# Performance work log

Hardware: AMD Instinct MI355X
Metric: run time of the kernel (lower is better)

Reference implementation:

```python
import jax, jax.numpy as jnp
import numpy as np

B, C, Hf, Wf, HM, P = 64, 2048, 16, 16, 256, 10  # P = num_parts, NP = graph nodes
NP = P - 1
EPS = 1e-5  # BatchNorm eps

def bn_eval(x, g, b, rm, rv):
    return (x - rm) * jax.lax.rsqrt(rv + EPS) * g + b

def setup_inputs() -> dict:
    key = jax.random.key(0)
    ks = jax.random.split(key, 6)
    return {
        "x_global": jax.random.normal(ks[0], (B, C, Hf, Wf), jnp.float32),
        "x_gcn": jax.random.normal(ks[1], (B, C, Hf, Wf), jnp.float32),
        "mask": jax.random.randint(ks[2], (B, 1, HM, HM), 0, P, jnp.int32),
        "adj": jax.random.uniform(ks[3], (B, NP, NP), jnp.float32),
        "W1": jax.random.normal(ks[4], (C, C), jnp.float32) * 0.02,
        "b1": jnp.zeros((C,), jnp.float32),
        "g1": jnp.ones((NP * C,), jnp.float32), "be1": jnp.zeros((NP * C,), jnp.float32),
        "rm1": jnp.zeros((NP * C,), jnp.float32), "rv1": jnp.ones((NP * C,), jnp.float32),
        "W2": jax.random.normal(ks[5], (C, C), jnp.float32) * 0.02,
        "b2": jnp.zeros((C,), jnp.float32),
        "g2": jnp.ones((NP * C,), jnp.float32), "be2": jnp.zeros((NP * C,), jnp.float32),
        "rm2": jnp.zeros((NP * C,), jnp.float32), "rv2": jnp.ones((NP * C,), jnp.float32),
        "gb_g": jnp.ones((C,), jnp.float32), "gb_b": jnp.zeros((C,), jnp.float32),
        "gb_rm": jnp.zeros((C,), jnp.float32), "gb_rv": jnp.ones((C,), jnp.float32),
        "gn_g": jnp.ones((C,), jnp.float32), "gn_b": jnp.zeros((C,), jnp.float32),
        "gn_rm": jnp.zeros((C,), jnp.float32), "gn_rv": jnp.ones((C,), jnp.float32),
    }

def gc_layer(x, adj, Wt, bias, g, be, rm, rv):
    # GraphConvolution: matmul -> bmm(adj) -> bias -> BN over flattened (B, NP*C)
    s = jnp.einsum('bpc,cd->bpd', x, Wt)
    o = jnp.einsum('bpq,bqd->bpd', adj, s) + bias
    flat = o.reshape(o.shape[0], -1)
    return bn_eval(flat, g, be, rm, rv).reshape(o.shape)

def reference(x_global, x_gcn, mask, adj, W1, b1, g1, be1, rm1, rv1,
              W2, b2, g2, be2, rm2, rv2, gb_g, gb_b, gb_rm, gb_rv,
              gn_g, gn_b, gn_rm, gn_rv):
    # --- global branch: GAP + bottleneck BN (eval) ---
    feat_global = x_global.mean(axis=(2, 3))                      # (B, C)
    bnfeat_global = bn_eval(feat_global, gb_g, gb_b, gb_rm, gb_rv)

    # --- nearest-neighbor downsample of mask to feature-map size ---
    stride = HM // Hf
    mr = mask[:, 0, ::stride, ::stride]                           # (B, h, w)

    # one-hot part masks for classes 1..P-1: (B, h, w, NP)
    onehot = (mr[..., None] == jnp.arange(1, P)).astype(jnp.float32)
    counts = onehot.sum(axis=(1, 2))                              # (B, NP)

    # deterministic part dropout: drop the first present part per image
    drop = jnp.argmax(counts > 0, axis=1) + 1                     # (B,)
    keep = (mr != drop[:, None, None]).astype(jnp.float32)        # (B, h, w)
    x_self = x_gcn * keep[:, None, :, :]

    # segment mean pooling per part: (B, NP, C)
    denom = (counts + 1e-8)[..., None]
    mask_feat = jnp.einsum('bchw,bhwp->bpc', x_gcn, onehot) / denom
    self_feat = jnp.einsum('bchw,bhwp->bpc', x_self, onehot) / denom

    def gcn(x):
        x1 = jax.nn.relu(gc_layer(x, adj, W1, b1, g1, be1, rm1, rv1))
        x2 = jax.nn.relu(gc_layer(x1, adj, W2, b2, g2, be2, rm2, rv2))
        return x2.mean(axis=1), x2.reshape(x2.shape[0], -1)

    feat_gcn, feat_gcn_cat = gcn(mask_feat)
    feat_self, feat_self_cat = gcn(self_feat)
    bnfeat_gcn = bn_eval(feat_gcn, gn_g, gn_b, gn_rm, gn_rv)
    bnfeat_self = bn_eval(feat_self, gn_g, gn_b, gn_rm, gn_rv)

    # concatenate eval-mode outputs into one array: (B, 3*C + 2*NP*C)
    return jnp.concatenate([bnfeat_global, bnfeat_gcn, bnfeat_self,
                            feat_gcn_cat, feat_self_cat], axis=1)
```

## Files before the change

kernel.cpp:

```cpp
#include <hip/hip_runtime.h>
#include <cstdint>
#include <cstddef>

#define EPSV 1e-5f

typedef __bf16 bf16x8 __attribute__((ext_vector_type(8)));
typedef float f32x4 __attribute__((ext_vector_type(4)));

__device__ __forceinline__ unsigned short f2bf(float f) {
  unsigned int u = __float_as_uint(f);
  u += 0x7FFFu + ((u >> 16) & 1u);
  return (unsigned short)(u >> 16);
}

__device__ __forceinline__ void async_copy16(const void* src, void* dst_lds) {
  __builtin_amdgcn_global_load_lds(
      (const __attribute__((address_space(1))) void*)src,
      (__attribute__((address_space(3))) void*)dst_lds, 16, 0, 0);
}

__global__ __launch_bounds__(256) void kmean(
    const float* __restrict__ x, const float* __restrict__ g,
    const float* __restrict__ bb, const float* __restrict__ rm,
    const float* __restrict__ rv, float* __restrict__ out) {
  int gw = blockIdx.x * 4 + (threadIdx.x >> 6);
  int lane = threadIdx.x & 63;
  float4 v = ((const float4*)(x + (size_t)gw * 256))[lane];
  float s = v.x + v.y + v.z + v.w;
#pragma unroll
  for (int o = 32; o > 0; o >>= 1) s += __shfl_xor(s, o, 64);
  if (lane == 0) {
    int b = gw >> 11, c = gw & 2047;
    float m = s * (1.f / 256.f);
    out[(size_t)b * 43008 + c] =
        (m - rm[c]) / sqrtf(rv[c] + EPSV) * g[c] + bb[c];
  }
}

__global__ __launch_bounds__(256) void kmask(
    const int* __restrict__ mask, int* __restrict__ partid,
    float* __restrict__ invden, int* __restrict__ dropm1) {
  int b = blockIdx.x;
  int t = threadIdx.x;
  int h = t >> 4, w = t & 15;
  int m = mask[(size_t)b * 65536 + h * 4096 + w * 16];
  partid[b * 256 + t] = m;
  __shared__ int cnt[10];
  if (t < 10) cnt[t] = 0;
  __syncthreads();
  atomicAdd(&cnt[m], 1);
  __syncthreads();
  if (t == 0) {
    int dp = 0;
    for (int p = 8; p >= 0; p--)
      if (cnt[p + 1] > 0) dp = p;
    dropm1[b] = dp;
  }
  if (t < 9) invden[b * 9 + t] = 1.f / ((float)cnt[t + 1] + 1e-8f);
}

__global__ __launch_bounds__(256) void kpool_mfma(
    const float* __restrict__ x, const int* __restrict__ partid,
    const float* __restrict__ invden, const int* __restrict__ dropm1,
    unsigned short* __restrict__ Abuf) {
  __shared__ unsigned short As[64 * 264];
  __shared__ unsigned short Bs[16 * 264];
  __shared__ int pid[256];
  const int t = threadIdx.x;
  const int b = blockIdx.y;
  const int c0 = blockIdx.x * 64;

  pid[t] = partid[b * 256 + t];

  const float4* xg = (const float4*)(x + ((size_t)(b * 2048 + c0)) * 256);
#pragma unroll
  for (int it = 0; it < 16; it++) {
    int idx = t + it * 256;
    float4 v = xg[idx];
    int row = idx >> 6, sc = (idx & 63) * 4;
    ushort4 h;
    h.x = f2bf(v.x); h.y = f2bf(v.y); h.z = f2bf(v.z); h.w = f2bf(v.w);
    *(ushort4*)&As[row * 264 + sc] = h;
  }
  __syncthreads();
  {
    int p = t >> 4, s0 = (t & 15) * 16;
#pragma unroll
    for (int j = 0; j < 16; j++)
      Bs[p * 264 + s0 + j] =
          (pid[s0 + j] == p + 1) ? (unsigned short)0x3F80 : (unsigned short)0;
  }
  __syncthreads();

  const int wave = t >> 6;
  const int l16 = t & 15;
  const int quad = (t & 63) >> 4;
  f32x4 acc = (f32x4){0.f, 0.f, 0.f, 0.f};
#pragma unroll
  for (int ks = 0; ks < 8; ks++) {
    bf16x8 a = *(const bf16x8*)&As[(wave * 16 + l16) * 264 + ks * 32 + quad * 8];
    bf16x8 bf = *(const bf16x8*)&Bs[l16 * 264 + ks * 32 + quad * 8];
    acc = __builtin_amdgcn_mfma_f32_16x16x32_bf16(a, bf, acc, 0, 0, 0);
  }

  if (l16 < 9) {
    int p = l16;
    float inv = invden[b * 9 + p];
    int dm1 = dropm1[b];
    int cbase = c0 + wave * 16 + quad * 4;
    ushort4 hm;
    hm.x = f2bf(acc[0] * inv);
    hm.y = f2bf(acc[1] * inv);
    hm.z = f2bf(acc[2] * inv);
    hm.w = f2bf(acc[3] * inv);
    ushort4 hs = (p == dm1) ? (ushort4){0, 0, 0, 0} : hm;
    *(ushort4*)&Abuf[(size_t)(b * 9 + p) * 2048 + cbase] = hm;
    *(ushort4*)&Abuf[(size_t)((64 + b) * 9 + p) * 2048 + cbase] = hs;
  }
}

__global__ __launch_bounds__(256) void ktranspose(
    const float* __restrict__ W1, const float* __restrict__ W2,
    unsigned short* __restrict__ Wt1, unsigned short* __restrict__ Wt2) {
  const float* W = blockIdx.z ? W2 : W1;
  unsigned short* Wt = blockIdx.z ? Wt2 : Wt1;
  __shared__ float tile[32][33];
  int tx = threadIdx.x & 31;
  int ty = threadIdx.x >> 5;
  int k0 = blockIdx.y * 32;
  int n0 = blockIdx.x * 32;
#pragma unroll
  for (int i = 0; i < 32; i += 8)
    tile[ty + i][tx] = W[(size_t)(k0 + ty + i) * 2048 + n0 + tx];
  __syncthreads();
#pragma unroll
  for (int i = 0; i < 32; i += 8)
    Wt[(size_t)(n0 + ty + i) * 2048 + k0 + tx] = f2bf(tile[tx][ty + i]);
}

#define GK 2048
__global__ __launch_bounds__(256) void gemm_bf16(
    const unsigned short* __restrict__ A, const unsigned short* __restrict__ Bt,
    float* __restrict__ S) {
  __shared__ unsigned short As[128 * 32];
  __shared__ unsigned short Bs[128 * 32];
  const int tid = threadIdx.x;
  const int lane = tid & 63;
  const int wave = tid >> 6;
  const int wm = (wave >> 1) << 6;
  const int wn = (wave & 1) << 6;
  const int quad = lane >> 4;
  const int l16 = lane & 15;
  const int by = blockIdx.y;
  const int bx = blockIdx.x;
  const int kz = blockIdx.z;

  const unsigned short* Ag = A + (size_t)by * 128 * GK;
  const unsigned short* Bg = Bt + (size_t)bx * 128 * GK;
  S += (size_t)kz * 1152 * 2048;

  f32x4 acc[4][4];
#pragma unroll
  for (int i = 0; i < 4; i++)
#pragma unroll
    for (int j = 0; j < 4; j++) acc[i][j] = (f32x4){0.f, 0.f, 0.f, 0.f};

  const int seg0 = tid, seg1 = tid + 256;
  const int r0 = seg0 >> 2, c0 = (seg0 & 3) * 8;
  const int r1 = seg1 >> 2, c1 = (seg1 & 3) * 8;

  const int kbeg = kz * (GK / 2), kend = kbeg + (GK / 2);
  for (int kk = kbeg; kk < kend; kk += 32) {
    __syncthreads();
    async_copy16(Ag + (size_t)r0 * GK + kk + c0, &As[seg0 * 8]);
    async_copy16(Ag + (size_t)r1 * GK + kk + c1, &As[seg1 * 8]);
    async_copy16(Bg + (size_t)r0 * GK + kk + c0, &Bs[seg0 * 8]);
    async_copy16(Bg + (size_t)r1 * GK + kk + c1, &Bs[seg1 * 8]);
    asm volatile("s_waitcnt vmcnt(0)" ::: "memory");
    __syncthreads();

    bf16x8 af[4], bfr[4];
#pragma unroll
    for (int i = 0; i < 4; i++)
      af[i] = *(const bf16x8*)&As[(wm + i * 16 + l16) * 32 + quad * 8];
#pragma unroll
    for (int j = 0; j < 4; j++)
      bfr[j] = *(const bf16x8*)&Bs[(wn + j * 16 + l16) * 32 + quad * 8];
#pragma unroll
    for (int i = 0; i < 4; i++)
#pragma unroll
      for (int j = 0; j < 4; j++)
        acc[i][j] = __builtin_amdgcn_mfma_f32_16x16x32_bf16(af[i], bfr[j],
                                                            acc[i][j], 0, 0, 0);
  }

#pragma unroll
  for (int i = 0; i < 4; i++)
#pragma unroll
    for (int j = 0; j < 4; j++)
#pragma unroll
      for (int r = 0; r < 4; r++) {
        int m = by * 128 + wm + i * 16 + quad * 4 + r;
        int n = bx * 128 + wn + j * 16 + l16;
        S[(size_t)m * 2048 + n] = acc[i][j][r];
      }
}

__global__ __launch_bounds__(256) void epi_mid(
    const float* __restrict__ S0, const float* __restrict__ S1,
    const float* __restrict__ adj, const float* __restrict__ bias,
    const float* __restrict__ g, const float* __restrict__ be,
    const float* __restrict__ rm, const float* __restrict__ rv,
    unsigned short* __restrict__ Aout) {
  int idx = blockIdx.x * 256 + threadIdx.x;
  int d = idx & 2047;
  int bb = idx >> 11;
  int b = bb & 63;
  float s[9];
#pragma unroll
  for (int q = 0; q < 9; q++) {
    size_t off = (size_t)(bb * 9 + q) * 2048 + d;
    s[q] = S0[off] + S1[off];
  }
#pragma unroll
  for (int p = 0; p < 9; p++) {
    float o = bias[d];
#pragma unroll
    for (int q = 0; q < 9; q++) o += adj[b * 81 + p * 9 + q] * s[q];
    int f = p * 2048 + d;
    float v = (o - rm[f]) / sqrtf(rv[f] + EPSV) * g[f] + be[f];
    v = fmaxf(v, 0.f);
    Aout[(size_t)(bb * 9 + p) * 2048 + d] = f2bf(v);
  }
}

__global__ __launch_bounds__(256) void epi_final(
    const float* __restrict__ S0, const float* __restrict__ S1,
    const float* __restrict__ adj, const float* __restrict__ bias,
    const float* __restrict__ g, const float* __restrict__ be,
    const float* __restrict__ rm, const float* __restrict__ rv,
    const float* __restrict__ gn_g, const float* __restrict__ gn_b,
    const float* __restrict__ gn_rm, const float* __restrict__ gn_rv,
    float* __restrict__ out) {
  int idx = blockIdx.x * 256 + threadIdx.x;
  int d = idx & 2047;
  int bb = idx >> 11;
  int b = bb & 63;
  bool selfb = bb >= 64;
  float s[9];
#pragma unroll
  for (int q = 0; q < 9; q++) {
    size_t off = (size_t)(bb * 9 + q) * 2048 + d;
    s[q] = S0[off] + S1[off];
  }
  float* orow = out + (size_t)b * 43008;
  size_t catbase = selfb ? 24576 : 6144;
  float mean = 0.f;
#pragma unroll
  for (int p = 0; p < 9; p++) {
    float o = bias[d];
#pragma unroll
    for (int q = 0; q < 9; q++) o += adj[b * 81 + p * 9 + q] * s[q];
    int f = p * 2048 + d;
    float v = (o - rm[f]) / sqrtf(rv[f] + EPSV) * g[f] + be[f];
    v = fmaxf(v, 0.f);
    mean += v;
    orow[catbase + f] = v;
  }
  mean *= (1.f / 9.f);
  orow[(selfb ? 4096 : 2048) + d] =
      (mean - gn_rm[d]) / sqrtf(gn_rv[d] + EPSV) * gn_g[d] + gn_b[d];
}

extern "C" void kernel_launch(void* const* d_in, const int* in_sizes, int n_in,
                              void* d_out, int out_size, void* d_ws,
                              size_t ws_size, hipStream_t stream) {
  const float* x_global = (const float*)d_in[0];
  const float* x_gcn = (const float*)d_in[1];
  const int* mask = (const int*)d_in[2];
  const float* adj = (const float*)d_in[3];
  const float* W1 = (const float*)d_in[4];
  const float* b1 = (const float*)d_in[5];
  const float* g1 = (const float*)d_in[6];
  const float* be1 = (const float*)d_in[7];
  const float* rm1 = (const float*)d_in[8];
  const float* rv1 = (const float*)d_in[9];
  const float* W2 = (const float*)d_in[10];
  const float* b2 = (const float*)d_in[11];
  const float* g2 = (const float*)d_in[12];
  const float* be2 = (const float*)d_in[13];
  const float* rm2 = (const float*)d_in[14];
  const float* rv2 = (const float*)d_in[15];
  const float* gb_g = (const float*)d_in[16];
  const float* gb_b = (const float*)d_in[17];
  const float* gb_rm = (const float*)d_in[18];
  const float* gb_rv = (const float*)d_in[19];
  const float* gn_g = (const float*)d_in[20];
  const float* gn_b = (const float*)d_in[21];
  const float* gn_rm = (const float*)d_in[22];
  const float* gn_rv = (const float*)d_in[23];
  float* out = (float*)d_out;

  char* ws = (char*)d_ws;
  int* partid = (int*)(ws);
  float* invden = (float*)(ws + 65536);
  int* dropm1 = (int*)(ws + 67840);
  unsigned short* Abuf = (unsigned short*)(ws + 131072);
  unsigned short* Wt1 = (unsigned short*)(ws + 131072 + 4718592);
  unsigned short* Wt2 =
      (unsigned short*)(ws + 131072 + 4718592 + 8388608);
  float* S0 = (float*)(ws + 131072 + 4718592 + 2 * 8388608);
  float* S1 = S0 + (size_t)1152 * 2048;

  ktranspose<<<dim3(64, 64, 2), 256, 0, stream>>>(W1, W2, Wt1, Wt2);
  kmean<<<32768, 256, 0, stream>>>(x_global, gb_g, gb_b, gb_rm, gb_rv, out);
  kmask<<<64, 256, 0, stream>>>(mask, partid, invden, dropm1);
  kpool_mfma<<<dim3(32, 64), 256, 0, stream>>>(x_gcn, partid, invden, dropm1,
                                               Abuf);
  gemm_bf16<<<dim3(16, 9, 2), 256, 0, stream>>>(Abuf, Wt1, S0);
  epi_mid<<<1024, 256, 0, stream>>>(S0, S1, adj, b1, g1, be1, rm1, rv1, Abuf);
  gemm_bf16<<<dim3(16, 9, 2), 256, 0, stream>>>(Abuf, Wt2, S0);
  epi_final<<<1024, 256, 0, stream>>>(S0, S1, adj, b2, g2, be2, rm2, rv2, gn_g,
                                      gn_b, gn_rm, gn_rv, out);
}
```

Measured before the change: 429.5 us.

## Double-buffer GEMM with swizzled LDS, split-K by 4, merge prep kernels

```diff
diff --git a/kernel.cpp b/kernel.cpp
--- a/kernel.cpp
+++ b/kernel.cpp
@@ -19,44 +19,64 @@
       (__attribute__((address_space(3))) void*)dst_lds, 16, 0, 0);
 }
 
-__global__ __launch_bounds__(256) void kmean(
-    const float* __restrict__ x, const float* __restrict__ g,
-    const float* __restrict__ bb, const float* __restrict__ rm,
-    const float* __restrict__ rv, float* __restrict__ out) {
-  int gw = blockIdx.x * 4 + (threadIdx.x >> 6);
-  int lane = threadIdx.x & 63;
-  float4 v = ((const float4*)(x + (size_t)gw * 256))[lane];
-  float s = v.x + v.y + v.z + v.w;
-#pragma unroll
-  for (int o = 32; o > 0; o >>= 1) s += __shfl_xor(s, o, 64);
-  if (lane == 0) {
-    int b = gw >> 11, c = gw & 2047;
-    float m = s * (1.f / 256.f);
-    out[(size_t)b * 43008 + c] =
-        (m - rm[c]) / sqrtf(rv[c] + EPSV) * g[c] + bb[c];
-  }
-}
-
-__global__ __launch_bounds__(256) void kmask(
+__global__ __launch_bounds__(256) void prep(
+    const float* __restrict__ W1, const float* __restrict__ W2,
+    unsigned short* __restrict__ Wt1, unsigned short* __restrict__ Wt2,
+    const float* __restrict__ xg, const float* __restrict__ gb_g,
+    const float* __restrict__ gb_b, const float* __restrict__ gb_rm,
+    const float* __restrict__ gb_rv, float* __restrict__ out,
     const int* __restrict__ mask, int* __restrict__ partid,
     float* __restrict__ invden, int* __restrict__ dropm1) {
-  int b = blockIdx.x;
-  int t = threadIdx.x;
-  int h = t >> 4, w = t & 15;
-  int m = mask[(size_t)b * 65536 + h * 4096 + w * 16];
-  partid[b * 256 + t] = m;
-  __shared__ int cnt[10];
-  if (t < 10) cnt[t] = 0;
-  __syncthreads();
-  atomicAdd(&cnt[m], 1);
-  __syncthreads();
-  if (t == 0) {
-    int dp = 0;
-    for (int p = 8; p >= 0; p--)
-      if (cnt[p + 1] > 0) dp = p;
-    dropm1[b] = dp;
-  }
-  if (t < 9) invden[b * 9 + t] = 1.f / ((float)cnt[t + 1] + 1e-8f);
+  int blk = blockIdx.x;
+  if (blk < 8192) {
+    int z = blk >> 12;
+    int rem = blk & 4095;
+    int by = rem >> 6, bx = rem & 63;
+    const float* W = z ? W2 : W1;
+    unsigned short* Wt = z ? Wt2 : Wt1;
+    __shared__ float tile[32][33];
+    int tx = threadIdx.x & 31;
+    int ty = threadIdx.x >> 5;
+    int k0 = by * 32, n0 = bx * 32;
+#pragma unroll
+    for (int i = 0; i < 32; i += 8)
+      tile[ty + i][tx] = W[(size_t)(k0 + ty + i) * 2048 + n0 + tx];
+    __syncthreads();
+#pragma unroll
+    for (int i = 0; i < 32; i += 8)
+      Wt[(size_t)(n0 + ty + i) * 2048 + k0 + tx] = f2bf(tile[tx][ty + i]);
+  } else if (blk < 40960) {
+    int gw = (blk - 8192) * 4 + (threadIdx.x >> 6);
+    int lane = threadIdx.x & 63;
+    float4 v = ((const float4*)(xg + (size_t)gw * 256))[lane];
+    float s = v.x + v.y + v.z + v.w;
+#pragma unroll
+    for (int o = 32; o > 0; o >>= 1) s += __shfl_xor(s, o, 64);
+    if (lane == 0) {
+      int b = gw >> 11, c = gw & 2047;
+      float m = s * (1.f / 256.f);
+      out[(size_t)b * 43008 + c] =
+          (m - gb_rm[c]) / sqrtf(gb_rv[c] + EPSV) * gb_g[c] + gb_b[c];
+    }
+  } else {
+    int b = blk - 40960;
+    int t = threadIdx.x;
+    int h = t >> 4, w = t & 15;
+    int m = mask[(size_t)b * 65536 + h * 4096 + w * 16];
+    partid[b * 256 + t] = m;
+    __shared__ int cnt[10];
+    if (t < 10) cnt[t] = 0;
+    __syncthreads();
+    atomicAdd(&cnt[m], 1);
+    __syncthreads();
+    if (t == 0) {
+      int dp = 0;
+      for (int p = 8; p >= 0; p--)
+        if (cnt[p + 1] > 0) dp = p;
+      dropm1[b] = dp;
+    }
+    if (t < 9) invden[b * 9 + t] = 1.f / ((float)cnt[t + 1] + 1e-8f);
+  }
 }
 
 __global__ __launch_bounds__(256) void kpool_mfma(
@@ -72,11 +92,11 @@
 
   pid[t] = partid[b * 256 + t];
 
-  const float4* xg = (const float4*)(x + ((size_t)(b * 2048 + c0)) * 256);
+  const float4* xgp = (const float4*)(x + ((size_t)(b * 2048 + c0)) * 256);
 #pragma unroll
   for (int it = 0; it < 16; it++) {
     int idx = t + it * 256;
-    float4 v = xg[idx];
+    float4 v = xgp[idx];
     int row = idx >> 6, sc = (idx & 63) * 4;
     ushort4 h;
     h.x = f2bf(v.x); h.y = f2bf(v.y); h.z = f2bf(v.z); h.w = f2bf(v.w);
@@ -119,31 +139,13 @@
   }
 }
 
-__global__ __launch_bounds__(256) void ktranspose(
-    const float* __restrict__ W1, const float* __restrict__ W2,
-    unsigned short* __restrict__ Wt1, unsigned short* __restrict__ Wt2) {
-  const float* W = blockIdx.z ? W2 : W1;
-  unsigned short* Wt = blockIdx.z ? Wt2 : Wt1;
-  __shared__ float tile[32][33];
-  int tx = threadIdx.x & 31;
-  int ty = threadIdx.x >> 5;
-  int k0 = blockIdx.y * 32;
-  int n0 = blockIdx.x * 32;
-#pragma unroll
-  for (int i = 0; i < 32; i += 8)
-    tile[ty + i][tx] = W[(size_t)(k0 + ty + i) * 2048 + n0 + tx];
-  __syncthreads();
-#pragma unroll
-  for (int i = 0; i < 32; i += 8)
-    Wt[(size_t)(n0 + ty + i) * 2048 + k0 + tx] = f2bf(tile[tx][ty + i]);
-}
-
 #define GK 2048
-__global__ __launch_bounds__(256) void gemm_bf16(
+#define SPART (1152 * 2048)
+__global__ __launch_bounds__(256) void gemm_db(
     const unsigned short* __restrict__ A, const unsigned short* __restrict__ Bt,
     float* __restrict__ S) {
-  __shared__ unsigned short As[128 * 32];
-  __shared__ unsigned short Bs[128 * 32];
+  __shared__ unsigned short As[2][128 * 64];
+  __shared__ unsigned short Bs[2][128 * 64];
   const int tid = threadIdx.x;
   const int lane = tid & 63;
   const int wave = tid >> 6;
@@ -157,7 +159,7 @@
 
   const unsigned short* Ag = A + (size_t)by * 128 * GK;
   const unsigned short* Bg = Bt + (size_t)bx * 128 * GK;
-  S += (size_t)kz * 1152 * 2048;
+  S += (size_t)kz * SPART;
 
   f32x4 acc[4][4];
 #pragma unroll
@@ -165,33 +167,65 @@
 #pragma unroll
     for (int j = 0; j < 4; j++) acc[i][j] = (f32x4){0.f, 0.f, 0.f, 0.f};
 
-  const int seg0 = tid, seg1 = tid + 256;
-  const int r0 = seg0 >> 2, c0 = (seg0 & 3) * 8;
-  const int r1 = seg1 >> 2, c1 = (seg1 & 3) * 8;
-
-  const int kbeg = kz * (GK / 2), kend = kbeg + (GK / 2);
-  for (int kk = kbeg; kk < kend; kk += 32) {
-    __syncthreads();
-    async_copy16(Ag + (size_t)r0 * GK + kk + c0, &As[seg0 * 8]);
-    async_copy16(Ag + (size_t)r1 * GK + kk + c1, &As[seg1 * 8]);
-    async_copy16(Bg + (size_t)r0 * GK + kk + c0, &Bs[seg0 * 8]);
-    async_copy16(Bg + (size_t)r1 * GK + kk + c1, &Bs[seg1 * 8]);
-    asm volatile("s_waitcnt vmcnt(0)" ::: "memory");
-    __syncthreads();
-
-    bf16x8 af[4], bfr[4];
-#pragma unroll
-    for (int i = 0; i < 4; i++)
-      af[i] = *(const bf16x8*)&As[(wm + i * 16 + l16) * 32 + quad * 8];
-#pragma unroll
-    for (int j = 0; j < 4; j++)
-      bfr[j] = *(const bf16x8*)&Bs[(wn + j * 16 + l16) * 32 + quad * 8];
-#pragma unroll
-    for (int i = 0; i < 4; i++)
-#pragma unroll
-      for (int j = 0; j < 4; j++)
-        acc[i][j] = __builtin_amdgcn_mfma_f32_16x16x32_bf16(af[i], bfr[j],
-                                                            acc[i][j], 0, 0, 0);
+  int srow[4], scol[4];
+#pragma unroll
+  for (int s = 0; s < 4; s++) {
+    int idx = tid + s * 256;
+    srow[s] = idx >> 3;
+    scol[s] = ((idx & 7) ^ (srow[s] & 7)) * 8;
+  }
+
+  const int kbeg = kz * 512;
+
+#define STAGE(buf, kk)                                                        \
+  do {                                                                        \
+    _Pragma("unroll") for (int s = 0; s < 4; s++) {                           \
+      int idx = tid + s * 256;                                                \
+      async_copy16(Ag + (size_t)srow[s] * GK + (kk) + scol[s],                \
+                   &As[buf][idx * 8]);                                        \
+    }                                                                         \
+    _Pragma("unroll") for (int s = 0; s < 4; s++) {                           \
+      int idx = tid + s * 256;                                                \
+      async_copy16(Bg + (size_t)srow[s] * GK + (kk) + scol[s],                \
+                   &Bs[buf][idx * 8]);                                        \
+    }                                                                         \
+  } while (0)
+
+  STAGE(0, kbeg);
+  asm volatile("s_waitcnt vmcnt(0)" ::: "memory");
+  __syncthreads();
+
+  for (int it = 0; it < 8; it++) {
+    const int cur = it & 1;
+    if (it < 7) STAGE(cur ^ 1, kbeg + (it + 1) * 64);
+
+#pragma unroll
+    for (int ks = 0; ks < 2; ks++) {
+      bf16x8 af[4], bfr[4];
+#pragma unroll
+      for (int i = 0; i < 4; i++) {
+        int row = wm + i * 16 + l16;
+        int slot = row * 8 + ((ks * 4 + quad) ^ (row & 7));
+        af[i] = *(const bf16x8*)&As[cur][slot * 8];
+      }
+#pragma unroll
+      for (int j = 0; j < 4; j++) {
+        int row = wn + j * 16 + l16;
+        int slot = row * 8 + ((ks * 4 + quad) ^ (row & 7));
+        bfr[j] = *(const bf16x8*)&Bs[cur][slot * 8];
+      }
+#pragma unroll
+      for (int i = 0; i < 4; i++)
+#pragma unroll
+        for (int j = 0; j < 4; j++)
+          acc[i][j] = __builtin_amdgcn_mfma_f32_16x16x32_bf16(
+              af[i], bfr[j], acc[i][j], 0, 0, 0);
+    }
+
+    if (it < 7) {
+      asm volatile("s_waitcnt vmcnt(0)" ::: "memory");
+      __syncthreads();
+    }
   }
 
 #pragma unroll
@@ -207,11 +241,10 @@
 }
 
 __global__ __launch_bounds__(256) void epi_mid(
-    const float* __restrict__ S0, const float* __restrict__ S1,
-    const float* __restrict__ adj, const float* __restrict__ bias,
-    const float* __restrict__ g, const float* __restrict__ be,
-    const float* __restrict__ rm, const float* __restrict__ rv,
-    unsigned short* __restrict__ Aout) {
+    const float* __restrict__ S, const float* __restrict__ adj,
+    const float* __restrict__ bias, const float* __restrict__ g,
+    const float* __restrict__ be, const float* __restrict__ rm,
+    const float* __restrict__ rv, unsigned short* __restrict__ Aout) {
   int idx = blockIdx.x * 256 + threadIdx.x;
   int d = idx & 2047;
   int bb = idx >> 11;
@@ -220,7 +253,7 @@
 #pragma unroll
   for (int q = 0; q < 9; q++) {
     size_t off = (size_t)(bb * 9 + q) * 2048 + d;
-    s[q] = S0[off] + S1[off];
+    s[q] = S[off] + S[off + SPART] + S[off + 2 * SPART] + S[off + 3 * SPART];
   }
 #pragma unroll
   for (int p = 0; p < 9; p++) {
@@ -235,13 +268,12 @@
 }
 
 __global__ __launch_bounds__(256) void epi_final(
-    const float* __restrict__ S0, const float* __restrict__ S1,
-    const float* __restrict__ adj, const float* __restrict__ bias,
-    const float* __restrict__ g, const float* __restrict__ be,
-    const float* __restrict__ rm, const float* __restrict__ rv,
-    const float* __restrict__ gn_g, const float* __restrict__ gn_b,
-    const float* __restrict__ gn_rm, const float* __restrict__ gn_rv,
-    float* __restrict__ out) {
+    const float* __restrict__ S, const float* __restrict__ adj,
+    const float* __restrict__ bias, const float* __restrict__ g,
+    const float* __restrict__ be, const float* __restrict__ rm,
+    const float* __restrict__ rv, const float* __restrict__ gn_g,
+    const float* __restrict__ gn_b, const float* __restrict__ gn_rm,
+    const float* __restrict__ gn_rv, float* __restrict__ out) {
   int idx = blockIdx.x * 256 + threadIdx.x;
   int d = idx & 2047;
   int bb = idx >> 11;
@@ -251,7 +283,7 @@
 #pragma unroll
   for (int q = 0; q < 9; q++) {
     size_t off = (size_t)(bb * 9 + q) * 2048 + d;
-    s[q] = S0[off] + S1[off];
+    s[q] = S[off] + S[off + SPART] + S[off + 2 * SPART] + S[off + 3 * SPART];
   }
   float* orow = out + (size_t)b * 43008;
   size_t catbase = selfb ? 24576 : 6144;
@@ -306,20 +338,18 @@
   float* invden = (float*)(ws + 65536);
   int* dropm1 = (int*)(ws + 67840);
   unsigned short* Abuf = (unsigned short*)(ws + 131072);
-  unsigned short* Wt1 = (unsigned short*)(ws + 131072 + 4718592);
-  unsigned short* Wt2 =
-      (unsigned short*)(ws + 131072 + 4718592 + 8388608);
-  float* S0 = (float*)(ws + 131072 + 4718592 + 2 * 8388608);
-  float* S1 = S0 + (size_t)1152 * 2048;
-
-  ktranspose<<<dim3(64, 64, 2), 256, 0, stream>>>(W1, W2, Wt1, Wt2);
-  kmean<<<32768, 256, 0, stream>>>(x_global, gb_g, gb_b, gb_rm, gb_rv, out);
-  kmask<<<64, 256, 0, stream>>>(mask, partid, invden, dropm1);
+  unsigned short* Wt1 = (unsigned short*)(ws + 4849664);
+  unsigned short* Wt2 = (unsigned short*)(ws + 13238272);
+  float* S = (float*)(ws + 21626880);
+
+  prep<<<41024, 256, 0, stream>>>(W1, W2, Wt1, Wt2, x_global, gb_g, gb_b,
+                                  gb_rm, gb_rv, out, mask, partid, invden,
+                                  dropm1);
   kpool_mfma<<<dim3(32, 64), 256, 0, stream>>>(x_gcn, partid, invden, dropm1,
                                                Abuf);
-  gemm_bf16<<<dim3(16, 9, 2), 256, 0, stream>>>(Abuf, Wt1, S0);
-  epi_mid<<<1024, 256, 0, stream>>>(S0, S1, adj, b1, g1, be1, rm1, rv1, Abuf);
-  gemm_bf16<<<dim3(16, 9, 2), 256, 0, stream>>>(Abuf, Wt2, S0);
-  epi_final<<<1024, 256, 0, stream>>>(S0, S1, adj, b2, g2, be2, rm2, rv2, gn_g,
+  gemm_db<<<dim3(16, 9, 4), 256, 0, stream>>>(Abuf, Wt1, S);
+  epi_mid<<<1024, 256, 0, stream>>>(S, adj, b1, g1, be1, rm1, rv1, Abuf);
+  gemm_db<<<dim3(16, 9, 4), 256, 0, stream>>>(Abuf, Wt2, S);
+  epi_final<<<1024, 256, 0, stream>>>(S, adj, b2, g2, be2, rm2, rv2, gn_g,
                                       gn_b, gn_rm, gn_rv, out);
 }
```

Result: faster. 411.1 us (-4.3%).
